# Kernel optimization log

Measured on AMD Instinct MI355X. Metric: run time of the kernel, lower is better.

## Reference

```python
import jax, jax.numpy as jnp
import numpy as np

B, F, V, D, A, ND = 4096, 26, 100000, 16, 16, 13


def setup_inputs() -> dict:
    key = jax.random.key(0)
    ks = jax.random.split(key, 10)
    dense_input = jax.random.normal(ks[0], (B, ND), dtype=jnp.float32)
    sparse_input = jax.random.randint(ks[1], (B, F), 0, V, dtype=jnp.int32)
    # all fields share feat_num=V, so stack tables into one [F, V, D] array
    embed_tables = jax.random.normal(ks[2], (F, V, D), dtype=jnp.float32) * 0.001
    att_W = jax.random.normal(ks[3], (D, A), dtype=jnp.float32) * (2.0 / (D + A)) ** 0.5
    att_b = jnp.zeros((A,), dtype=jnp.float32)
    att_h = jax.random.normal(ks[4], (A, 1), dtype=jnp.float32) * (2.0 / (A + 1)) ** 0.5
    att_p = jax.random.normal(ks[5], (D, 1), dtype=jnp.float32) * (2.0 / (D + 1)) ** 0.5
    lin_w_dense = jax.random.normal(ks[6], (ND, 1), dtype=jnp.float32) * 0.01
    lin_w_sparse = jax.random.normal(ks[7], (F * D, 1), dtype=jnp.float32) * 0.01
    lin_b = jnp.zeros((1,), dtype=jnp.float32)
    return {"dense_input": dense_input, "sparse_input": sparse_input,
            "embed_tables": embed_tables, "att_W": att_W, "att_b": att_b,
            "att_h": att_h, "att_p": att_p, "lin_w_dense": lin_w_dense,
            "lin_w_sparse": lin_w_sparse, "lin_b": lin_b}


def reference(dense_input, sparse_input, embed_tables, att_W, att_b, att_h,
              att_p, lin_w_dense, lin_w_sparse, lin_b):
    # per-field embedding gather: [B, F, D]
    emb = embed_tables[jnp.arange(F)[None, :], sparse_input]
    sparse_concat = emb.reshape(B, F * D)
    # linear part (Linear(dense, sparse_concat) -> [B, 1])
    linear_result = dense_input @ lin_w_dense + sparse_concat @ lin_w_sparse + lin_b
    # pairwise element-wise products for i < j: [B, P, D], P = F*(F-1)/2
    iu, ju = np.triu_indices(F, k=1)
    ewp = emb[:, iu, :] * emb[:, ju, :]
    # attention MLP over pairs
    att_wx_b = jax.nn.relu(jnp.einsum('bpd,da->bpa', ewp, att_W) + att_b)
    score = jax.nn.softmax(jnp.einsum('bpa,ao->bpo', att_wx_b, att_h), axis=1)  # [B,P,1]
    att_output = jnp.sum(score * ewp, axis=1)  # [B, D]; dropout_rate=0 -> identity
    afm_result = att_output @ att_p  # [B, 1]
    return jax.nn.sigmoid(afm_result + linear_result)
```

## Files before the change

kernel.cpp:

```cpp
#include <hip/hip_runtime.h>
#include <hip/hip_bf16.h>

typedef float  v2f    __attribute__((ext_vector_type(2)));
typedef float  f32x16 __attribute__((ext_vector_type(16)));
typedef _Float16 half8 __attribute__((ext_vector_type(8)));
typedef _Float16 half4v __attribute__((ext_vector_type(4)));

#define BATCH 4096
#define NF 26
#define NV 100000
#define ND_ 16
#define NA 16
#define NDENSE 13
#define NPAIR 325
#define ROWH 24
#define WPB 4
#define BLOCK 512
#define SCALE 256.0f
#define INV_SCALE2 (1.0f / 65536.0f)

__global__ __launch_bounds__(BLOCK, 8) void afm_kernel(
    const float* __restrict__ dense,
    const int*   __restrict__ sparse,
    const float* __restrict__ tables,
    const float* __restrict__ attW,
    const float* __restrict__ attB,
    const float* __restrict__ attH,
    const float* __restrict__ attP,
    const float* __restrict__ wDense,
    const float* __restrict__ wSparse,
    const float* __restrict__ linB,
    float* __restrict__ out)
{
    __shared__ int sOFF[NPAIR];
    __shared__ __align__(16) _Float16 sEmbH[WPB][NF * ROWH];
    __shared__ float sPart[WPB][2][3];

    const int tid  = threadIdx.x;
    const int wave = tid >> 6;
    const int lane = tid & 63;
    const int item = wave >> 1;
    const int subw = wave & 1;
    const int col  = lane & 31;
    const int hi   = lane >> 5;
    const int b    = blockIdx.x * WPB + item;

    int idxreg = 0;
    if (lane < NF) idxreg = sparse[b * NF + lane];

    float lin = 0.f;
    {
        const int c = subw * 64 + lane;
        if (c < (NF * ND_) / 4) {
            const int f  = c >> 2;
            const int d4 = (c & 3) << 2;
            const int row = __shfl(idxreg, f);
            const float4 v = *reinterpret_cast<const float4*>(
                tables + ((size_t)f * NV + (size_t)row) * ND_ + d4);
            const float4 w = *reinterpret_cast<const float4*>(wSparse + f * ND_ + d4);
            lin += v.x * w.x + v.y * w.y + v.z * w.z + v.w * w.w;
            half4v hv;
            hv[0] = (_Float16)(v.x * SCALE);
            hv[1] = (_Float16)(v.y * SCALE);
            hv[2] = (_Float16)(v.z * SCALE);
            hv[3] = (_Float16)(v.w * SCALE);
            *reinterpret_cast<half4v*>(&sEmbH[item][f * ROWH + d4]) = hv;
        }
    }
    if (subw == 0 && lane < NDENSE)
        lin += dense[b * NDENSE + lane] * wDense[lane];

    if (tid < NPAIR) {
        int i = 0, rem = tid;
        while (rem >= NF - 1 - i) { rem -= NF - 1 - i; ++i; }
        const int j = i + 1 + rem;
        sOFF[tid] = (i * ROWH) | ((j * ROWH) << 16);
    }

    half8 afrag;
    #pragma unroll
    for (int t = 0; t < 8; ++t) {
        float a = 0.f;
        if (col < NA)       a = attW[(hi * 8 + t) * NA + col];
        else if (col == NA) a = attP[hi * 8 + t];
        afrag[t] = (_Float16)a;
    }
    v2f h2[4], b2[4];
    #pragma unroll
    for (int r = 0; r < 8; ++r) {
        const int k = (r & 3) + 8 * (r >> 2) + 4 * hi;
        h2[r >> 1][r & 1] = attH[k] * INV_SCALE2;
        b2[r >> 1][r & 1] = attB[k] * 65536.0f;
    }

    __syncthreads();

    const _Float16* __restrict__ embH = sEmbH[item];

    float num = 0.f, den = 0.f;
    auto tiles = [&](const int t0, const int NT) {
        #pragma unroll
        for (int tt = 0; tt < NT; ++tt) {
            const int t     = t0 + tt;
            const int p     = t * 32 + col;
            const bool valid = (p < NPAIR) && (hi == 0);
            const int pc    = (p < NPAIR) ? p : (NPAIR - 1);
            const int offs  = sOFF[pc];

            const half8 ai = *reinterpret_cast<const half8*>(embH + (offs & 0xffff) + hi * 8);
            const half8 aj = *reinterpret_cast<const half8*>(embH + (offs >> 16)    + hi * 8);
            const half8 bfrag = ai * aj;

            f32x16 acc = {0.f,0.f,0.f,0.f,0.f,0.f,0.f,0.f,
                          0.f,0.f,0.f,0.f,0.f,0.f,0.f,0.f};
            acc = __builtin_amdgcn_mfma_f32_32x32x16_f16(afrag, bfrag, acc, 0, 0, 0);

            v2f sp2 = {0.f, 0.f};
            #pragma unroll
            for (int r = 0; r < 4; ++r) {
                v2f z; z.x = acc[2 * r]; z.y = acc[2 * r + 1];
                z = z + b2[r];
                v2f zr; zr.x = fmaxf(z.x, 0.f); zr.y = fmaxf(z.y, 0.f);
                sp2 = zr * h2[r] + sp2;
            }
            const float sp = sp2.x + sp2.y;
            const float sfull = sp + __shfl_xor(sp, 32);

            const float ev = valid ? __expf(sfull) : 0.f;
            num = fmaf(ev, acc[8], num);
            den += ev;
        }
    };
    if (subw == 0) tiles(0, 6); else tiles(6, 5);

    #pragma unroll
    for (int o = 32; o; o >>= 1) {
        num += __shfl_xor(num, o);
        den += __shfl_xor(den, o);
        lin += __shfl_xor(lin, o);
    }
    if (lane == 0) {
        sPart[item][subw][0] = num;
        sPart[item][subw][1] = den;
        sPart[item][subw][2] = lin;
    }
    __syncthreads();

    if (subw == 0 && lane == 0) {
        const float n = sPart[item][0][0] + sPart[item][1][0];
        const float d = sPart[item][0][1] + sPart[item][1][1];
        const float l = sPart[item][0][2] + sPart[item][1][2];
        const float x = (n * INV_SCALE2) / d + l + linB[0];
        out[b] = 1.f / (1.f + __expf(-x));
    }
}

extern "C" void kernel_launch(void* const* d_in, const int* in_sizes, int n_in,
                              void* d_out, int out_size, void* d_ws, size_t ws_size,
                              hipStream_t stream) {
    const float* dense   = (const float*)d_in[0];
    const int*   sparse  = (const int*)d_in[1];
    const float* tables  = (const float*)d_in[2];
    const float* attW    = (const float*)d_in[3];
    const float* attB    = (const float*)d_in[4];
    const float* attH    = (const float*)d_in[5];
    const float* attP    = (const float*)d_in[6];
    const float* wDense  = (const float*)d_in[7];
    const float* wSparse = (const float*)d_in[8];
    const float* linB    = (const float*)d_in[9];
    float* out = (float*)d_out;

    const int grid = BATCH / WPB;
    afm_kernel<<<grid, BLOCK, 0, stream>>>(
        dense, sparse, tables, attW, attB, attH, attP,
        wDense, wSparse, linB, out);
}
```

Before: 13.45 us.

## Process two batch items per wave group and prefetch second embedding gather

```diff
diff --git a/kernel.cpp b/kernel.cpp
--- a/kernel.cpp
+++ b/kernel.cpp
@@ -3,7 +3,7 @@
 
 typedef float  v2f    __attribute__((ext_vector_type(2)));
 typedef float  f32x16 __attribute__((ext_vector_type(16)));
-typedef _Float16 half8 __attribute__((ext_vector_type(8)));
+typedef _Float16 half8  __attribute__((ext_vector_type(8)));
 typedef _Float16 half4v __attribute__((ext_vector_type(4)));
 
 #define BATCH 4096
@@ -15,11 +15,12 @@
 #define NPAIR 325
 #define ROWH 24
 #define WPB 4
+#define ROUNDS 2
 #define BLOCK 512
 #define SCALE 256.0f
 #define INV_SCALE2 (1.0f / 65536.0f)
 
-__global__ __launch_bounds__(BLOCK, 8) void afm_kernel(
+__global__ __launch_bounds__(BLOCK, 4) void afm_kernel(
     const float* __restrict__ dense,
     const int*   __restrict__ sparse,
     const float* __restrict__ tables,
@@ -43,32 +44,34 @@
     const int subw = wave & 1;
     const int col  = lane & 31;
     const int hi   = lane >> 5;
-    const int b    = blockIdx.x * WPB + item;
-
-    int idxreg = 0;
-    if (lane < NF) idxreg = sparse[b * NF + lane];
-
-    float lin = 0.f;
-    {
-        const int c = subw * 64 + lane;
-        if (c < (NF * ND_) / 4) {
-            const int f  = c >> 2;
-            const int d4 = (c & 3) << 2;
-            const int row = __shfl(idxreg, f);
-            const float4 v = *reinterpret_cast<const float4*>(
-                tables + ((size_t)f * NV + (size_t)row) * ND_ + d4);
-            const float4 w = *reinterpret_cast<const float4*>(wSparse + f * ND_ + d4);
-            lin += v.x * w.x + v.y * w.y + v.z * w.z + v.w * w.w;
-            half4v hv;
-            hv[0] = (_Float16)(v.x * SCALE);
-            hv[1] = (_Float16)(v.y * SCALE);
-            hv[2] = (_Float16)(v.z * SCALE);
-            hv[3] = (_Float16)(v.w * SCALE);
-            *reinterpret_cast<half4v*>(&sEmbH[item][f * ROWH + d4]) = hv;
-        }
-    }
-    if (subw == 0 && lane < NDENSE)
-        lin += dense[b * NDENSE + lane] * wDense[lane];
+    const int base = blockIdx.x * (WPB * ROUNDS);
+    const int b0   = base + item;
+    const int b1   = base + WPB + item;
+
+    int idx0 = 0, idx1 = 0;
+    if (lane < NF) {
+        idx0 = sparse[b0 * NF + lane];
+        idx1 = sparse[b1 * NF + lane];
+    }
+    float dn0 = 0.f, dn1 = 0.f, wD = 0.f;
+    if (subw == 0 && lane < NDENSE) {
+        dn0 = dense[b0 * NDENSE + lane];
+        dn1 = dense[b1 * NDENSE + lane];
+        wD  = wDense[lane];
+    }
+
+    const int c    = subw * 64 + lane;
+    const bool gact = c < (NF * ND_) / 4;
+    const int gf   = c >> 2;
+    const int gd4  = (c & 3) << 2;
+
+    float4 v0 = {0.f, 0.f, 0.f, 0.f}, w4 = {0.f, 0.f, 0.f, 0.f};
+    if (gact) {
+        const int row0 = __shfl(idx0, gf);
+        v0 = *reinterpret_cast<const float4*>(
+            tables + ((size_t)gf * NV + (size_t)row0) * ND_ + gd4);
+        w4 = *reinterpret_cast<const float4*>(wSparse + gf * ND_ + gd4);
+    }
 
     if (tid < NPAIR) {
         int i = 0, rem = tid;
@@ -93,12 +96,28 @@
         b2[r >> 1][r & 1] = attB[k] * 65536.0f;
     }
 
+    float lin0 = 0.f;
+    if (gact) {
+        lin0 = v0.x * w4.x + v0.y * w4.y + v0.z * w4.z + v0.w * w4.w;
+        half4v hv;
+        hv[0] = (_Float16)(v0.x * SCALE); hv[1] = (_Float16)(v0.y * SCALE);
+        hv[2] = (_Float16)(v0.z * SCALE); hv[3] = (_Float16)(v0.w * SCALE);
+        *reinterpret_cast<half4v*>(&sEmbH[item][gf * ROWH + gd4]) = hv;
+    }
+    if (subw == 0 && lane < NDENSE) lin0 += dn0 * wD;
+
+    float4 v1 = {0.f, 0.f, 0.f, 0.f};
+    if (gact) {
+        const int row1 = __shfl(idx1, gf);
+        v1 = *reinterpret_cast<const float4*>(
+            tables + ((size_t)gf * NV + (size_t)row1) * ND_ + gd4);
+    }
+
     __syncthreads();
 
     const _Float16* __restrict__ embH = sEmbH[item];
 
-    float num = 0.f, den = 0.f;
-    auto tiles = [&](const int t0, const int NT) {
+    auto tiles = [&](const int t0, const int NT, float& num, float& den) {
         #pragma unroll
         for (int tt = 0; tt < NT; ++tt) {
             const int t     = t0 + tt;
@@ -131,27 +150,65 @@
             den += ev;
         }
     };
-    if (subw == 0) tiles(0, 6); else tiles(6, 5);
-
-    #pragma unroll
-    for (int o = 32; o; o >>= 1) {
-        num += __shfl_xor(num, o);
-        den += __shfl_xor(den, o);
-        lin += __shfl_xor(lin, o);
-    }
-    if (lane == 0) {
-        sPart[item][subw][0] = num;
-        sPart[item][subw][1] = den;
-        sPart[item][subw][2] = lin;
-    }
-    __syncthreads();
-
+
+    {
+        float num = 0.f, den = 0.f, lin = lin0;
+        if (subw == 0) tiles(0, 6, num, den); else tiles(6, 5, num, den);
+        #pragma unroll
+        for (int o = 32; o; o >>= 1) {
+            num += __shfl_xor(num, o);
+            den += __shfl_xor(den, o);
+            lin += __shfl_xor(lin, o);
+        }
+        if (lane == 0) {
+            sPart[item][subw][0] = num;
+            sPart[item][subw][1] = den;
+            sPart[item][subw][2] = lin;
+        }
+    }
+    __syncthreads();
     if (subw == 0 && lane == 0) {
         const float n = sPart[item][0][0] + sPart[item][1][0];
         const float d = sPart[item][0][1] + sPart[item][1][1];
         const float l = sPart[item][0][2] + sPart[item][1][2];
         const float x = (n * INV_SCALE2) / d + l + linB[0];
-        out[b] = 1.f / (1.f + __expf(-x));
+        out[b0] = 1.f / (1.f + __expf(-x));
+    }
+
+    float lin1 = 0.f;
+    if (gact) {
+        lin1 = v1.x * w4.x + v1.y * w4.y + v1.z * w4.z + v1.w * w4.w;
+        half4v hv;
+        hv[0] = (_Float16)(v1.x * SCALE); hv[1] = (_Float16)(v1.y * SCALE);
+        hv[2] = (_Float16)(v1.z * SCALE); hv[3] = (_Float16)(v1.w * SCALE);
+        *reinterpret_cast<half4v*>(&sEmbH[item][gf * ROWH + gd4]) = hv;
+    }
+    if (subw == 0 && lane < NDENSE) lin1 += dn1 * wD;
+
+    __syncthreads();
+
+    {
+        float num = 0.f, den = 0.f, lin = lin1;
+        if (subw == 0) tiles(0, 6, num, den); else tiles(6, 5, num, den);
+        #pragma unroll
+        for (int o = 32; o; o >>= 1) {
+            num += __shfl_xor(num, o);
+            den += __shfl_xor(den, o);
+            lin += __shfl_xor(lin, o);
+        }
+        if (lane == 0) {
+            sPart[item][subw][0] = num;
+            sPart[item][subw][1] = den;
+            sPart[item][subw][2] = lin;
+        }
+    }
+    __syncthreads();
+    if (subw == 0 && lane == 0) {
+        const float n = sPart[item][0][0] + sPart[item][1][0];
+        const float d = sPart[item][0][1] + sPart[item][1][1];
+        const float l = sPart[item][0][2] + sPart[item][1][2];
+        const float x = (n * INV_SCALE2) / d + l + linB[0];
+        out[b1] = 1.f / (1.f + __expf(-x));
     }
 }
 
@@ -170,7 +227,7 @@
     const float* linB    = (const float*)d_in[9];
     float* out = (float*)d_out;
 
-    const int grid = BATCH / WPB;
+    const int grid = BATCH / (WPB * ROUNDS);
     afm_kernel<<<grid, BLOCK, 0, stream>>>(
         dense, sparse, tables, attW, attB, attH, attP,
         wDense, wSparse, linB, out);
```

Result: slower. 14.24 us (+5.9%).
